# Kernel optimization log

Hardware: AMD Instinct MI355X
Metric: run time of the kernel (lower is better)

The kernel has to match this reference:

```python
import jax, jax.numpy as jnp
import numpy as np

CLASS_NUM = 6
N = 8388608


def setup_inputs() -> dict:
    key = jax.random.key(0)
    k1, k2, k3 = jax.random.split(key, 3)
    inputs = jax.random.normal(k1, (N, CLASS_NUM), dtype=jnp.float32)
    targets = jax.random.randint(k2, (N, 1), 0, CLASS_NUM, dtype=jnp.int32)
    # learned parameter: torch.rand(class_num) -> uniform [0,1)
    class_weight = jax.random.uniform(k3, (CLASS_NUM,), dtype=jnp.float32)
    return {"inputs": inputs, "targets": targets, "class_weight": class_weight}


def reference(inputs, targets, class_weight):
    # weighted argmax over classes: [N]
    preds = jnp.argmax(class_weight * inputs, axis=-1)
    tgt = targets.reshape(-1)  # [N]
    # confusion_matrix[pred, target] += 1  (data-dependent scatter-add histogram)
    cm = jnp.zeros((CLASS_NUM, CLASS_NUM), dtype=jnp.float32)
    cm = cm.at[preds, tgt].add(1.0)
    precision = jnp.diag(cm) / cm.sum(axis=0)
    recall = jnp.diag(cm) / cm.sum(axis=1)
    f1 = 2.0 * precision * recall / (precision + recall)
    loss = -f1.mean()
    return (loss, class_weight)
```

## Files before the change

### kernel.cpp

```cpp
#include <hip/hip_runtime.h>

#define CLS 6

constexpr int HIST_BLOCKS  = 2048;
constexpr int HIST_THREADS = 256;
constexpr int NCOPY        = 4;
constexpr int CM_STRIDE    = 40;

__device__ __forceinline__ int argmax6(float v0, float v1, float v2,
                                       float v3, float v4, float v5) {
    int   pr = 0; float m = v0;
    if (v1 > m) { m = v1; pr = 1; }
    if (v2 > m) { m = v2; pr = 2; }
    if (v3 > m) { m = v3; pr = 3; }
    if (v4 > m) { m = v4; pr = 4; }
    if (v5 > m) { m = v5; pr = 5; }
    return pr;
}

__global__ __launch_bounds__(HIST_THREADS, 8)
void cm_hist_kernel(const float* __restrict__ inputs,
                    const int*   __restrict__ targets,
                    const float* __restrict__ wts,
                    unsigned int* __restrict__ cm,
                    long long n_rows) {
    __shared__ unsigned int cm_s[NCOPY * CM_STRIDE];
    const int tid = threadIdx.x;
    if (tid < NCOPY * CM_STRIDE) cm_s[tid] = 0u;
    __syncthreads();

    const float w0 = wts[0], w1 = wts[1], w2 = wts[2];
    const float w3 = wts[3], w4 = wts[4], w5 = wts[5];

    const float4* __restrict__ in4 = (const float4*)inputs;
    const int4*   __restrict__ tg4 = (const int4*)targets;

    const int copy_base = (tid & (NCOPY - 1)) * CM_STRIDE;

    const long long n_quads = n_rows >> 2;
    const long long stride  = (long long)gridDim.x * blockDim.x;

    for (long long q = (long long)blockIdx.x * blockDim.x + tid;
         q < n_quads; q += stride) {
        const long long b = 6 * q;
        float4 f0 = in4[b + 0];
        float4 f1 = in4[b + 1];
        float4 f2 = in4[b + 2];
        float4 f3 = in4[b + 3];
        float4 f4 = in4[b + 4];
        float4 f5 = in4[b + 5];
        int4   t  = tg4[q];

        int p0 = argmax6(f0.x * w0, f0.y * w1, f0.z * w2, f0.w * w3, f1.x * w4, f1.y * w5);
        int p1 = argmax6(f1.z * w0, f1.w * w1, f2.x * w2, f2.y * w3, f2.z * w4, f2.w * w5);
        int p2 = argmax6(f3.x * w0, f3.y * w1, f3.z * w2, f3.w * w3, f4.x * w4, f4.y * w5);
        int p3 = argmax6(f4.z * w0, f4.w * w1, f5.x * w2, f5.y * w3, f5.z * w4, f5.w * w5);

        atomicAdd(&cm_s[copy_base + p0 * CLS + t.x], 1u);
        atomicAdd(&cm_s[copy_base + p1 * CLS + t.y], 1u);
        atomicAdd(&cm_s[copy_base + p2 * CLS + t.z], 1u);
        atomicAdd(&cm_s[copy_base + p3 * CLS + t.w], 1u);
    }

    if (blockIdx.x == 0 && tid == 0) {
        for (long long r = (n_quads << 2); r < n_rows; ++r) {
            int pr = argmax6(inputs[r * CLS + 0] * w0, inputs[r * CLS + 1] * w1,
                             inputs[r * CLS + 2] * w2, inputs[r * CLS + 3] * w3,
                             inputs[r * CLS + 4] * w4, inputs[r * CLS + 5] * w5);
            atomicAdd(&cm_s[pr * CLS + targets[r]], 1u);
        }
    }

    __syncthreads();
    if (tid < CLS * CLS) {
        unsigned int v = cm_s[tid]
                       + cm_s[CM_STRIDE + tid]
                       + cm_s[2 * CM_STRIDE + tid]
                       + cm_s[3 * CM_STRIDE + tid];
        if (v) atomicAdd(&cm[tid], v);
    }
}

__global__ void macro_score_kernel(const unsigned int* __restrict__ cm,
                                   const float* __restrict__ wts,
                                   float* __restrict__ out) {
    if (threadIdx.x == 0) {
        float c[CLS * CLS];
        #pragma unroll
        for (int i = 0; i < CLS * CLS; ++i) c[i] = (float)cm[i];
        float f1sum = 0.0f;
        #pragma unroll
        for (int i = 0; i < CLS; ++i) {
            float col = 0.0f, row = 0.0f;
            #pragma unroll
            for (int j = 0; j < CLS; ++j) {
                col += c[j * CLS + i];
                row += c[i * CLS + j];
            }
            float d  = c[i * CLS + i];
            float pr = d / col;
            float rc = d / row;
            f1sum += 2.0f * pr * rc / (pr + rc);
        }
        out[0] = -(f1sum / (float)CLS);
    }
    if (threadIdx.x < CLS) out[1 + threadIdx.x] = wts[threadIdx.x];
}

extern "C" void kernel_launch(void* const* d_in, const int* in_sizes, int n_in,
                              void* d_out, int out_size, void* d_ws, size_t ws_size,
                              hipStream_t stream) {
    const float* inputs  = (const float*)d_in[0];
    const int*   targets = (const int*)d_in[1];
    const float* wts     = (const float*)d_in[2];
    float*       out     = (float*)d_out;
    unsigned int* cm     = (unsigned int*)d_ws;

    const long long n_rows = (long long)in_sizes[0] / CLS;

    (void)hipMemsetAsync(cm, 0, CLS * CLS * sizeof(unsigned int), stream);
    cm_hist_kernel<<<HIST_BLOCKS, HIST_THREADS, 0, stream>>>(inputs, targets, wts, cm, n_rows);
    macro_score_kernel<<<1, 64, 0, stream>>>(cm, wts, out);
}
```

Before: 300.2 us.

## Stage input rows through per-wave LDS for fully coalesced float4 loads

Each wave now loads a 64-quad chunk of inputs with lane-contiguous float4 reads, transposes it through a padded per-wave shared-memory buffer (stride 7), then reads back each lane's 6 float4s for argmax. This replaces the previous stride-96-byte per-thread global access pattern, which leaves each wave instruction touching scattered addresses. It adds LDS traffic and about 28 KB of shared memory per block, and lowers the launch-bounds occupancy hint from 8 to 5. A scalar tail loop handles leftover quads.

```diff
diff --git a/kernel.cpp b/kernel.cpp
--- a/kernel.cpp
+++ b/kernel.cpp
@@ -4,6 +4,7 @@
 
 constexpr int HIST_BLOCKS  = 2048;
 constexpr int HIST_THREADS = 256;
+constexpr int WAVES_PB     = HIST_THREADS / 64;
 constexpr int NCOPY        = 4;
 constexpr int CM_STRIDE    = 40;
 
@@ -18,14 +19,18 @@
     return pr;
 }
 
-__global__ __launch_bounds__(HIST_THREADS, 8)
+__global__ __launch_bounds__(HIST_THREADS, 5)
 void cm_hist_kernel(const float* __restrict__ inputs,
                     const int*   __restrict__ targets,
                     const float* __restrict__ wts,
                     unsigned int* __restrict__ cm,
                     long long n_rows) {
+    __shared__ float4       stage[WAVES_PB][64 * 7];
     __shared__ unsigned int cm_s[NCOPY * CM_STRIDE];
-    const int tid = threadIdx.x;
+
+    const int tid  = threadIdx.x;
+    const int wave = tid >> 6;
+    const int lane = tid & 63;
     if (tid < NCOPY * CM_STRIDE) cm_s[tid] = 0u;
     __syncthreads();
 
@@ -37,25 +42,63 @@
 
     const int copy_base = (tid & (NCOPY - 1)) * CM_STRIDE;
 
-    const long long n_quads = n_rows >> 2;
-    const long long stride  = (long long)gridDim.x * blockDim.x;
+    const long long n_quads  = n_rows >> 2;
+    const long long n_chunks = n_quads >> 6;
 
-    for (long long q = (long long)blockIdx.x * blockDim.x + tid;
-         q < n_quads; q += stride) {
-        const long long b = 6 * q;
-        float4 f0 = in4[b + 0];
-        float4 f1 = in4[b + 1];
-        float4 f2 = in4[b + 2];
-        float4 f3 = in4[b + 3];
-        float4 f4 = in4[b + 4];
-        float4 f5 = in4[b + 5];
-        int4   t  = tg4[q];
+    const long long wave_id = (long long)blockIdx.x * WAVES_PB + wave;
+    const long long n_waves = (long long)gridDim.x * WAVES_PB;
+
+    float4* st4 = &stage[wave][0];
+
+    for (long long c = wave_id; c < n_chunks; c += n_waves) {
+        const long long base_f4 = c * 384;
+
+        float4 r0 = in4[base_f4 +   0 + lane];
+        float4 r1 = in4[base_f4 +  64 + lane];
+        float4 r2 = in4[base_f4 + 128 + lane];
+        float4 r3 = in4[base_f4 + 192 + lane];
+        float4 r4 = in4[base_f4 + 256 + lane];
+        float4 r5 = in4[base_f4 + 320 + lane];
+        int4   t  = tg4[(c << 6) + lane];
+
+        {
+            unsigned u;
+            u = 0 * 64 + lane; st4[7 * (u / 6) + (u % 6)] = r0;
+            u = 1 * 64 + lane; st4[7 * (u / 6) + (u % 6)] = r1;
+            u = 2 * 64 + lane; st4[7 * (u / 6) + (u % 6)] = r2;
+            u = 3 * 64 + lane; st4[7 * (u / 6) + (u % 6)] = r3;
+            u = 4 * 64 + lane; st4[7 * (u / 6) + (u % 6)] = r4;
+            u = 5 * 64 + lane; st4[7 * (u / 6) + (u % 6)] = r5;
+        }
+
+        float4 f0 = st4[7 * lane + 0];
+        float4 f1 = st4[7 * lane + 1];
+        float4 f2 = st4[7 * lane + 2];
+        float4 f3 = st4[7 * lane + 3];
+        float4 f4 = st4[7 * lane + 4];
+        float4 f5 = st4[7 * lane + 5];
 
         int p0 = argmax6(f0.x * w0, f0.y * w1, f0.z * w2, f0.w * w3, f1.x * w4, f1.y * w5);
         int p1 = argmax6(f1.z * w0, f1.w * w1, f2.x * w2, f2.y * w3, f2.z * w4, f2.w * w5);
         int p2 = argmax6(f3.x * w0, f3.y * w1, f3.z * w2, f3.w * w3, f4.x * w4, f4.y * w5);
         int p3 = argmax6(f4.z * w0, f4.w * w1, f5.x * w2, f5.y * w3, f5.z * w4, f5.w * w5);
 
+        atomicAdd(&cm_s[copy_base + p0 * CLS + t.x], 1u);
+        atomicAdd(&cm_s[copy_base + p1 * CLS + t.y], 1u);
+        atomicAdd(&cm_s[copy_base + p2 * CLS + t.z], 1u);
+        atomicAdd(&cm_s[copy_base + p3 * CLS + t.w], 1u);
+    }
+
+    for (long long q = (n_chunks << 6) + (long long)blockIdx.x * blockDim.x + tid;
+         q < n_quads; q += (long long)gridDim.x * blockDim.x) {
+        const long long b = 6 * q;
+        float4 f0 = in4[b + 0], f1 = in4[b + 1], f2 = in4[b + 2];
+        float4 f3 = in4[b + 3], f4 = in4[b + 4], f5 = in4[b + 5];
+        int4   t  = tg4[q];
+        int p0 = argmax6(f0.x * w0, f0.y * w1, f0.z * w2, f0.w * w3, f1.x * w4, f1.y * w5);
+        int p1 = argmax6(f1.z * w0, f1.w * w1, f2.x * w2, f2.y * w3, f2.z * w4, f2.w * w5);
+        int p2 = argmax6(f3.x * w0, f3.y * w1, f3.z * w2, f3.w * w3, f4.x * w4, f4.y * w5);
+        int p3 = argmax6(f4.z * w0, f4.w * w1, f5.x * w2, f5.y * w3, f5.z * w4, f5.w * w5);
         atomicAdd(&cm_s[copy_base + p0 * CLS + t.x], 1u);
         atomicAdd(&cm_s[copy_base + p1 * CLS + t.y], 1u);
         atomicAdd(&cm_s[copy_base + p2 * CLS + t.z], 1u);
```

Measured after the change: 302.2 us. About the same (+0.7%).

## Prefetch next iteration's loads and replace global atomics with per-block partials

Applied to the files above, without the earlier changes.

The histogram loop now software-pipelines its work, issuing the next grid-stride iteration's vector loads before computing argmax and doing the shared atomics for the current one. Launch bounds drop from 8 to 4 waves per SIMD to leave room for the extra registers. Each block writes its 36-entry confusion matrix to a per-block slot in the workspace instead of using global atomics. This removes the memset, and a 1024-thread final kernel reduces all partials with wave shuffles. The cost is higher register pressure, lower occupancy, and a larger final reduction over 2048 partial rows.

```diff
diff --git a/kernel.cpp b/kernel.cpp
--- a/kernel.cpp
+++ b/kernel.cpp
@@ -6,6 +6,8 @@
 constexpr int HIST_THREADS = 256;
 constexpr int NCOPY        = 4;
 constexpr int CM_STRIDE    = 40;
+constexpr int CM_WORDS     = CLS * CLS;
+constexpr int PART_STRIDE  = CM_WORDS;
 
 __device__ __forceinline__ int argmax6(float v0, float v1, float v2,
                                        float v3, float v4, float v5) {
@@ -18,13 +20,13 @@
     return pr;
 }
 
-__global__ __launch_bounds__(HIST_THREADS, 8)
+__global__ __launch_bounds__(HIST_THREADS, 4)
 void cm_hist_kernel(const float* __restrict__ inputs,
                     const int*   __restrict__ targets,
                     const float* __restrict__ wts,
-                    unsigned int* __restrict__ cm,
+                    unsigned int* __restrict__ part,
                     long long n_rows) {
-    __shared__ unsigned int cm_s[NCOPY * CM_STRIDE];
+    __shared__ __align__(16) unsigned int cm_s[NCOPY * CM_STRIDE];
     const int tid = threadIdx.x;
     if (tid < NCOPY * CM_STRIDE) cm_s[tid] = 0u;
     __syncthreads();
@@ -40,26 +42,41 @@
     const long long n_quads = n_rows >> 2;
     const long long stride  = (long long)gridDim.x * blockDim.x;
 
-    for (long long q = (long long)blockIdx.x * blockDim.x + tid;
-         q < n_quads; q += stride) {
+    long long q = (long long)blockIdx.x * blockDim.x + tid;
+    bool have = q < n_quads;
+
+    float4 a0, a1, a2, a3, a4, a5; int4 at;
+    if (have) {
         const long long b = 6 * q;
-        float4 f0 = in4[b + 0];
-        float4 f1 = in4[b + 1];
-        float4 f2 = in4[b + 2];
-        float4 f3 = in4[b + 3];
-        float4 f4 = in4[b + 4];
-        float4 f5 = in4[b + 5];
-        int4   t  = tg4[q];
+        a0 = in4[b + 0]; a1 = in4[b + 1]; a2 = in4[b + 2];
+        a3 = in4[b + 3]; a4 = in4[b + 4]; a5 = in4[b + 5];
+        at = tg4[q];
+    }
 
-        int p0 = argmax6(f0.x * w0, f0.y * w1, f0.z * w2, f0.w * w3, f1.x * w4, f1.y * w5);
-        int p1 = argmax6(f1.z * w0, f1.w * w1, f2.x * w2, f2.y * w3, f2.z * w4, f2.w * w5);
-        int p2 = argmax6(f3.x * w0, f3.y * w1, f3.z * w2, f3.w * w3, f4.x * w4, f4.y * w5);
-        int p3 = argmax6(f4.z * w0, f4.w * w1, f5.x * w2, f5.y * w3, f5.z * w4, f5.w * w5);
+    while (have) {
+        const long long qn   = q + stride;
+        const bool      hvn  = qn < n_quads;
 
-        atomicAdd(&cm_s[copy_base + p0 * CLS + t.x], 1u);
-        atomicAdd(&cm_s[copy_base + p1 * CLS + t.y], 1u);
-        atomicAdd(&cm_s[copy_base + p2 * CLS + t.z], 1u);
-        atomicAdd(&cm_s[copy_base + p3 * CLS + t.w], 1u);
+        float4 b0, b1, b2, b3, b4, b5; int4 bt;
+        if (hvn) {
+            const long long b = 6 * qn;
+            b0 = in4[b + 0]; b1 = in4[b + 1]; b2 = in4[b + 2];
+            b3 = in4[b + 3]; b4 = in4[b + 4]; b5 = in4[b + 5];
+            bt = tg4[qn];
+        }
+
+        int p0 = argmax6(a0.x * w0, a0.y * w1, a0.z * w2, a0.w * w3, a1.x * w4, a1.y * w5);
+        int p1 = argmax6(a1.z * w0, a1.w * w1, a2.x * w2, a2.y * w3, a2.z * w4, a2.w * w5);
+        int p2 = argmax6(a3.x * w0, a3.y * w1, a3.z * w2, a3.w * w3, a4.x * w4, a4.y * w5);
+        int p3 = argmax6(a4.z * w0, a4.w * w1, a5.x * w2, a5.y * w3, a5.z * w4, a5.w * w5);
+
+        atomicAdd(&cm_s[copy_base + p0 * CLS + at.x], 1u);
+        atomicAdd(&cm_s[copy_base + p1 * CLS + at.y], 1u);
+        atomicAdd(&cm_s[copy_base + p2 * CLS + at.z], 1u);
+        atomicAdd(&cm_s[copy_base + p3 * CLS + at.w], 1u);
+
+        a0 = b0; a1 = b1; a2 = b2; a3 = b3; a4 = b4; a5 = b5; at = bt;
+        q = qn; have = hvn;
     }
 
     if (blockIdx.x == 0 && tid == 0) {
@@ -72,39 +89,72 @@
     }
 
     __syncthreads();
-    if (tid < CLS * CLS) {
-        unsigned int v = cm_s[tid]
-                       + cm_s[CM_STRIDE + tid]
-                       + cm_s[2 * CM_STRIDE + tid]
-                       + cm_s[3 * CM_STRIDE + tid];
-        if (v) atomicAdd(&cm[tid], v);
+    if (tid < CM_WORDS) {
+        cm_s[tid] = cm_s[tid]
+                  + cm_s[CM_STRIDE + tid]
+                  + cm_s[2 * CM_STRIDE + tid]
+                  + cm_s[3 * CM_STRIDE + tid];
+    }
+    __syncthreads();
+    if (tid < CM_WORDS / 4) {
+        ((uint4*)(part + (long long)blockIdx.x * PART_STRIDE))[tid] =
+            ((const uint4*)cm_s)[tid];
     }
 }
 
-__global__ void macro_score_kernel(const unsigned int* __restrict__ cm,
-                                   const float* __restrict__ wts,
-                                   float* __restrict__ out) {
-    if (threadIdx.x == 0) {
-        float c[CLS * CLS];
+__global__ __launch_bounds__(1024)
+void macro_score_kernel(const unsigned int* __restrict__ part,
+                        const float* __restrict__ wts,
+                        float* __restrict__ out) {
+    __shared__ float cmf_s[CM_WORDS];
+    const int tid  = threadIdx.x;
+    const int lane = tid & 63;
+    if (tid < CM_WORDS) cmf_s[tid] = 0.0f;
+    __syncthreads();
+
+    float acc[CM_WORDS];
+    #pragma unroll
+    for (int k = 0; k < CM_WORDS; ++k) acc[k] = 0.0f;
+
+    for (int r = tid; r < HIST_BLOCKS; r += 1024) {
+        const uint4* row = (const uint4*)(part + (long long)r * PART_STRIDE);
         #pragma unroll
-        for (int i = 0; i < CLS * CLS; ++i) c[i] = (float)cm[i];
+        for (int v = 0; v < CM_WORDS / 4; ++v) {
+            uint4 u = row[v];
+            acc[4 * v + 0] += (float)u.x;
+            acc[4 * v + 1] += (float)u.y;
+            acc[4 * v + 2] += (float)u.z;
+            acc[4 * v + 3] += (float)u.w;
+        }
+    }
+
+    #pragma unroll
+    for (int k = 0; k < CM_WORDS; ++k) {
+        float v = acc[k];
+        #pragma unroll
+        for (int off = 32; off > 0; off >>= 1) v += __shfl_down(v, off, 64);
+        if (lane == 0) atomicAdd(&cmf_s[k], v);
+    }
+    __syncthreads();
+
+    if (tid == 0) {
         float f1sum = 0.0f;
         #pragma unroll
         for (int i = 0; i < CLS; ++i) {
             float col = 0.0f, row = 0.0f;
             #pragma unroll
             for (int j = 0; j < CLS; ++j) {
-                col += c[j * CLS + i];
-                row += c[i * CLS + j];
+                col += cmf_s[j * CLS + i];
+                row += cmf_s[i * CLS + j];
             }
-            float d  = c[i * CLS + i];
+            float d  = cmf_s[i * CLS + i];
             float pr = d / col;
             float rc = d / row;
             f1sum += 2.0f * pr * rc / (pr + rc);
         }
         out[0] = -(f1sum / (float)CLS);
     }
-    if (threadIdx.x < CLS) out[1 + threadIdx.x] = wts[threadIdx.x];
+    if (tid < CLS) out[1 + tid] = wts[tid];
 }
 
 extern "C" void kernel_launch(void* const* d_in, const int* in_sizes, int n_in,
@@ -114,11 +164,10 @@
     const int*   targets = (const int*)d_in[1];
     const float* wts     = (const float*)d_in[2];
     float*       out     = (float*)d_out;
-    unsigned int* cm     = (unsigned int*)d_ws;
+    unsigned int* part   = (unsigned int*)d_ws;
 
     const long long n_rows = (long long)in_sizes[0] / CLS;
 
-    (void)hipMemsetAsync(cm, 0, CLS * CLS * sizeof(unsigned int), stream);
-    cm_hist_kernel<<<HIST_BLOCKS, HIST_THREADS, 0, stream>>>(inputs, targets, wts, cm, n_rows);
-    macro_score_kernel<<<1, 64, 0, stream>>>(cm, wts, out);
+    cm_hist_kernel<<<HIST_BLOCKS, HIST_THREADS, 0, stream>>>(inputs, targets, wts, part, n_rows);
+    macro_score_kernel<<<1, 1024, 0, stream>>>(part, wts, out);
 }
```

Result: slower. 316.3 us (+5.4%).
